# Kernel optimization log

Hardware: AMD Instinct MI355X
Metric: run time of the kernel (lower is better)

## Reference

```python
import jax, jax.numpy as jnp
import numpy as np

D_MODEL = 1024
N_HEADS = 16
D_K = D_MODEL // N_HEADS


def setup_inputs() -> dict:
    key = jax.random.key(0)
    ks = jax.random.split(key, 5)
    s = 1.0 / np.sqrt(D_MODEL)
    x = jax.random.normal(ks[0], (4, 2048, D_MODEL), dtype=jnp.float32)
    W_qkv = jax.random.normal(ks[1], (D_MODEL, 3 * D_MODEL), dtype=jnp.float32) * s
    b_qkv = jnp.zeros((3 * D_MODEL,), dtype=jnp.float32)
    W_proj = jax.random.normal(ks[2], (D_MODEL, D_MODEL), dtype=jnp.float32) * s
    b_proj = jnp.zeros((D_MODEL,), dtype=jnp.float32)
    return {"x": x, "W_qkv": W_qkv, "b_qkv": b_qkv, "W_proj": W_proj, "b_proj": b_proj}


def reference(x, W_qkv, b_qkv, W_proj, b_proj):
    B, T, C = x.shape
    qkv = x @ W_qkv + b_qkv  # [B,T,3C]
    q, k, v = jnp.split(qkv, 3, axis=2)
    # [B,T,C] -> [B,H,T,dk]
    def to_heads(t):
        return t.reshape(B, T, N_HEADS, D_K).transpose(0, 2, 1, 3)
    q, k, v = to_heads(q), to_heads(k), to_heads(v)
    scale = 1.0 / np.sqrt(D_K)
    att = jnp.einsum('bhqd,bhkd->bhqk', q, k) * scale
    causal = jnp.tril(jnp.ones((T, T), dtype=bool))
    att = jnp.where(causal, att, -jnp.inf)
    att = jax.nn.softmax(att, axis=-1)
    y = jnp.einsum('bhqk,bhkd->bhqd', att, v)
    y = y.transpose(0, 2, 1, 3).reshape(B, T, C)
    return y @ W_proj + b_proj
```

## Files before the change

### kernel.cpp

```cpp
#include <hip/hip_runtime.h>
#include <stdint.h>


typedef float  floatx4 __attribute__((ext_vector_type(4)));
typedef __bf16 bf16x8  __attribute__((ext_vector_type(8)));
typedef __bf16 bf16x4  __attribute__((ext_vector_type(4)));

#define AS1 __attribute__((address_space(1)))
#define AS3 __attribute__((address_space(3)))

__device__ __forceinline__ void gload_lds16(const void* g, void* l) {
    __builtin_amdgcn_global_load_lds((AS1 void*)(uintptr_t)g,
                                     (AS3 void*)(uintptr_t)l, 16, 0, 0);
}

#if __has_builtin(__builtin_amdgcn_exp2f)
#define EXP2F(x) __builtin_amdgcn_exp2f(x)
#else
#define EXP2F(x) exp2f(x)
#endif

#define LOG2E 1.44269504088896340736f
#define ATT_SC (0.125f * LOG2E)
#define MASK_NEG (-3.0e4f)

static constexpr int Bn = 4, Tn = 2048, Cn = 1024, Hn = 16, DKn = 64;
static constexpr int BT = Bn * Tn;
static constexpr int N_QKV = 3 * Cn;
static constexpr int PAD = 68;


__global__ void cast_x_kernel(const float* __restrict__ x, __bf16* __restrict__ xb, int n) {
    int i = (blockIdx.x * blockDim.x + threadIdx.x) * 4;
    if (i < n) {
        float4 v = *(const float4*)(x + i);
        bf16x4 o;
        o[0] = (__bf16)v.x; o[1] = (__bf16)v.y; o[2] = (__bf16)v.z; o[3] = (__bf16)v.w;
        *(bf16x4*)(xb + i) = o;
    }
}

__global__ void transpose_cast_kernel(const float* __restrict__ W, __bf16* __restrict__ WT,
                                      int R, int C) {
    __shared__ float tile[32][33];
    int tx = threadIdx.x & 31, ty = threadIdx.x >> 5;
    int r0 = blockIdx.y * 32, c0 = blockIdx.x * 32;
#pragma unroll
    for (int i = 0; i < 4; i++)
        tile[ty + i * 8][tx] = W[(size_t)(r0 + ty + i * 8) * C + c0 + tx];
    __syncthreads();
#pragma unroll
    for (int i = 0; i < 4; i++)
        WT[(size_t)(c0 + ty + i * 8) * R + r0 + tx] = (__bf16)tile[tx][ty + i * 8];
}

__global__ __launch_bounds__(256) void gemm_qkv_kernel(
    const __bf16* __restrict__ A, const __bf16* __restrict__ Bt,
    const float* __restrict__ bias,
    __bf16* __restrict__ Qo, __bf16* __restrict__ Ko, __bf16* __restrict__ Vo) {
    const int K = 1024;
    __shared__ __bf16 Al[128 * 32];
    __shared__ __bf16 Bl[128 * 32];
    int tid = threadIdx.x, w = tid >> 6, lane = tid & 63;
    int lq = lane >> 4, l16 = lane & 15;
    int bm = blockIdx.y, bn = blockIdx.x;
    int wm = w & 1, wn = w >> 1;

    const __bf16* Ag = A + (size_t)(bm * 128 + w * 32 + (lane >> 2)) * K + (lane & 3) * 8;
    const __bf16* Bg = Bt + (size_t)(bn * 128 + w * 32 + (lane >> 2)) * K + (lane & 3) * 8;
    __bf16* AlW = Al + w * 32 * 32;
    __bf16* BlW = Bl + w * 32 * 32;

    floatx4 acc[4][4] = {};
    for (int k0 = 0; k0 < K; k0 += 32) {
        __syncthreads();
        gload_lds16(Ag + k0, AlW);
        gload_lds16(Ag + k0 + 16 * K, AlW + 16 * 32);
        gload_lds16(Bg + k0, BlW);
        gload_lds16(Bg + k0 + 16 * K, BlW + 16 * 32);
        __syncthreads();
        bf16x8 af[4], bf[4];
#pragma unroll
        for (int i = 0; i < 4; i++)
            af[i] = *(const bf16x8*)&Al[(wm * 64 + i * 16 + l16) * 32 + lq * 8];
#pragma unroll
        for (int i = 0; i < 4; i++)
            bf[i] = *(const bf16x8*)&Bl[(wn * 64 + i * 16 + l16) * 32 + lq * 8];
#pragma unroll
        for (int mt = 0; mt < 4; mt++)
#pragma unroll
            for (int nt = 0; nt < 4; nt++)
                acc[mt][nt] = __builtin_amdgcn_mfma_f32_16x16x32_bf16(
                    af[mt], bf[nt], acc[mt][nt], 0, 0, 0);
    }
#pragma unroll
    for (int nt = 0; nt < 4; nt++) {
        int gbase = bn * 128 + wn * 64 + nt * 16;
        int gcol = gbase + l16;
        int which = gbase >> 10;
        float bv = bias[gcol];
        if (which == 2) {
            int hh = (gbase - 2048) >> 6;
            int dd = ((gbase - 2048) & 63) + l16;
#pragma unroll
            for (int mt = 0; mt < 4; mt++) {
                int growb = bm * 128 + wm * 64 + mt * 16 + lq * 4;
                int bb = growb >> 11, tt = growb & 2047;
                bf16x4 v4;
#pragma unroll
                for (int r = 0; r < 4; r++) v4[r] = (__bf16)(acc[mt][nt][r] + bv);
                *(bf16x4*)&Vo[((size_t)(bb * 16 + hh) * 64 + dd) * 2048 + tt] = v4;
            }
        } else {
            int rem = gbase & 1023;
            int hh = rem >> 6, dd = (rem & 63) + l16;
            __bf16* dst = (which == 0) ? Qo : Ko;
            float scl = (which == 0) ? ATT_SC : 1.0f;
#pragma unroll
            for (int mt = 0; mt < 4; mt++) {
#pragma unroll
                for (int r = 0; r < 4; r++) {
                    int grow = bm * 128 + wm * 64 + mt * 16 + lq * 4 + r;
                    int bb = grow >> 11, tt = grow & 2047;
                    dst[((size_t)(bb * 16 + hh) * 2048 + tt) * 64 + dd] =
                        (__bf16)((acc[mt][nt][r] + bv) * scl);
                }
            }
        }
    }
}

__global__ __launch_bounds__(256) void gemm_proj_kernel(
    const __bf16* __restrict__ A, const __bf16* __restrict__ Bt,
    const float* __restrict__ bias, float* __restrict__ out) {
    const int K = 1024;
    __shared__ __bf16 Al[128 * 32];
    __shared__ __bf16 Bl[128 * 32];
    int tid = threadIdx.x, w = tid >> 6, lane = tid & 63;
    int lq = lane >> 4, l16 = lane & 15;
    int bm = blockIdx.y, bn = blockIdx.x;
    int wm = w & 1, wn = w >> 1;

    const __bf16* Ag = A + (size_t)(bm * 128 + w * 32 + (lane >> 2)) * K + (lane & 3) * 8;
    const __bf16* Bg = Bt + (size_t)(bn * 128 + w * 32 + (lane >> 2)) * K + (lane & 3) * 8;
    __bf16* AlW = Al + w * 32 * 32;
    __bf16* BlW = Bl + w * 32 * 32;

    floatx4 acc[4][4] = {};
    for (int k0 = 0; k0 < K; k0 += 32) {
        __syncthreads();
        gload_lds16(Ag + k0, AlW);
        gload_lds16(Ag + k0 + 16 * K, AlW + 16 * 32);
        gload_lds16(Bg + k0, BlW);
        gload_lds16(Bg + k0 + 16 * K, BlW + 16 * 32);
        __syncthreads();
        bf16x8 af[4], bf[4];
#pragma unroll
        for (int i = 0; i < 4; i++)
            af[i] = *(const bf16x8*)&Al[(wm * 64 + i * 16 + l16) * 32 + lq * 8];
#pragma unroll
        for (int i = 0; i < 4; i++)
            bf[i] = *(const bf16x8*)&Bl[(wn * 64 + i * 16 + l16) * 32 + lq * 8];
#pragma unroll
        for (int mt = 0; mt < 4; mt++)
#pragma unroll
            for (int nt = 0; nt < 4; nt++)
                acc[mt][nt] = __builtin_amdgcn_mfma_f32_16x16x32_bf16(
                    af[mt], bf[nt], acc[mt][nt], 0, 0, 0);
    }
#pragma unroll
    for (int nt = 0; nt < 4; nt++) {
        int gcol = bn * 128 + wn * 64 + nt * 16 + l16;
        float bv = bias[gcol];
#pragma unroll
        for (int mt = 0; mt < 4; mt++) {
#pragma unroll
            for (int r = 0; r < 4; r++) {
                int grow = bm * 128 + wm * 64 + mt * 16 + lq * 4 + r;
                out[(size_t)grow * 1024 + gcol] = acc[mt][nt][r] + bv;
            }
        }
    }
}

__global__ __launch_bounds__(256) void attn_kernel(
    const __bf16* __restrict__ Q, const __bf16* __restrict__ K,
    const __bf16* __restrict__ Vt, __bf16* __restrict__ Y) {
    const int bid = blockIdx.x;
    const int pr = bid >> 6, bh = bid & 63;
    const int b = bh >> 4, h = bh & 15;
    int tid = threadIdx.x, w = tid >> 6, lane = tid & 63;
    int lq = lane >> 4, l16 = lane & 15;

    const __bf16* Qh = Q + (size_t)bh * Tn * DKn;
    const __bf16* Kh = K + (size_t)bh * Tn * DKn;
    const __bf16* Vh = Vt + (size_t)bh * DKn * Tn;

    __shared__ __bf16 Kl[64 * PAD];
    __shared__ __bf16 Vl[64 * PAD];
    __shared__ __bf16 Pl[128 * PAD];

    int srow = tid >> 3, ssl = tid & 7;

    bf16x8 onesf;
#pragma unroll
    for (int j = 0; j < 8; j++) onesf[j] = (__bf16)1.0f;

    bf16x8 kr0 = *(const bf16x8*)&Kh[(size_t)srow * 64 + ssl * 8];
    bf16x8 kr1 = *(const bf16x8*)&Kh[(size_t)(srow + 32) * 64 + ssl * 8];
    bf16x8 vr0 = *(const bf16x8*)&Vh[(size_t)srow * 2048 + ssl * 8];
    bf16x8 vr1 = *(const bf16x8*)&Vh[(size_t)(srow + 32) * 2048 + ssl * 8];

#pragma unroll
    for (int seg = 0; seg < 2; seg++) {
        const int qt = seg ? (15 - pr) : pr;
        const int q0 = qt * 128;
        const int ktmax = 2 * qt + 1;

        bf16x8 qf[2][2];
#pragma unroll
        for (int mt = 0; mt < 2; mt++)
#pragma unroll
            for (int ks = 0; ks < 2; ks++)
                qf[mt][ks] = *(const bf16x8*)&Qh[(size_t)(q0 + w * 32 + mt * 16 + l16) * 64 +
                                                 ks * 32 + lq * 8];

        floatx4 oacc[2][5] = {};

        for (int kt = 0; kt <= ktmax; kt++) {
            __syncthreads();
            *(bf16x8*)&Kl[srow * PAD + ssl * 8] = kr0;
            *(bf16x8*)&Kl[(srow + 32) * PAD + ssl * 8] = kr1;
            *(bf16x8*)&Vl[srow * PAD + ssl * 8] = vr0;
            *(bf16x8*)&Vl[(srow + 32) * PAD + ssl * 8] = vr1;
            __syncthreads();
            if (!(seg == 1 && kt == ktmax)) {
                int nk = (kt < ktmax) ? (kt + 1) : 0;
                kr0 = *(const bf16x8*)&Kh[(size_t)(nk * 64 + srow) * 64 + ssl * 8];
                kr1 = *(const bf16x8*)&Kh[(size_t)(nk * 64 + srow + 32) * 64 + ssl * 8];
                vr0 = *(const bf16x8*)&Vh[(size_t)srow * 2048 + nk * 64 + ssl * 8];
                vr1 = *(const bf16x8*)&Vh[(size_t)(srow + 32) * 2048 + nk * 64 + ssl * 8];
            }

            floatx4 s2[2][4] = {};
#pragma unroll
            for (int ks = 0; ks < 2; ks++) {
                bf16x8 kf[4];
#pragma unroll
                for (int nt = 0; nt < 4; nt++)
                    kf[nt] = *(const bf16x8*)&Kl[(nt * 16 + l16) * PAD + ks * 32 + lq * 8];
#pragma unroll
                for (int mt = 0; mt < 2; mt++)
#pragma unroll
                    for (int nt = 0; nt < 4; nt++)
                        s2[mt][nt] = __builtin_amdgcn_mfma_f32_16x16x32_bf16(
                            qf[mt][ks], kf[nt], s2[mt][nt], 0, 0, 0);
            }

            if (kt >= 2 * qt) {
#pragma unroll
                for (int mt = 0; mt < 2; mt++)
#pragma unroll
                    for (int nt = 0; nt < 4; nt++) {
                        int col = kt * 64 + nt * 16 + l16;
#pragma unroll
                        for (int r = 0; r < 4; r++) {
                            int row = q0 + w * 32 + mt * 16 + lq * 4 + r;
                            if (col > row) s2[mt][nt][r] = MASK_NEG;
                        }
                    }
            }

#pragma unroll
            for (int mt = 0; mt < 2; mt++) {
#pragma unroll
                for (int nt = 0; nt < 4; nt++) {
#pragma unroll
                    for (int r = 0; r < 4; r++) {
                        float p = EXP2F(s2[mt][nt][r]);
                        int rowl = w * 32 + mt * 16 + lq * 4 + r;
                        Pl[rowl * PAD + nt * 16 + l16] = (__bf16)p;
                    }
                }
            }

#pragma unroll
            for (int ks = 0; ks < 2; ks++) {
                bf16x8 pf[2], vf[4];
#pragma unroll
                for (int mt = 0; mt < 2; mt++)
                    pf[mt] = *(const bf16x8*)&Pl[(w * 32 + mt * 16 + l16) * PAD + ks * 32 + lq * 8];
#pragma unroll
                for (int dt = 0; dt < 4; dt++)
                    vf[dt] = *(const bf16x8*)&Vl[(dt * 16 + l16) * PAD + ks * 32 + lq * 8];
#pragma unroll
                for (int mt = 0; mt < 2; mt++) {
#pragma unroll
                    for (int dt = 0; dt < 4; dt++)
                        oacc[mt][dt] = __builtin_amdgcn_mfma_f32_16x16x32_bf16(
                            pf[mt], vf[dt], oacc[mt][dt], 0, 0, 0);
                    oacc[mt][4] = __builtin_amdgcn_mfma_f32_16x16x32_bf16(
                        pf[mt], onesf, oacc[mt][4], 0, 0, 0);
                }
            }
        }

#pragma unroll
        for (int mt = 0; mt < 2; mt++) {
#pragma unroll
            for (int r = 0; r < 4; r++) {
                float inv = 1.0f / oacc[mt][4][r];
                int rowg = q0 + w * 32 + mt * 16 + lq * 4 + r;
#pragma unroll
                for (int dt = 0; dt < 4; dt++)
                    Y[((size_t)(b * 2048 + rowg)) * 1024 + h * 64 + dt * 16 + l16] =
                        (__bf16)(oacc[mt][dt][r] * inv);
            }
        }
    }
}


extern "C" void kernel_launch(void* const* d_in, const int* in_sizes, int n_in,
                              void* d_out, int out_size, void* d_ws, size_t ws_size,
                              hipStream_t stream) {
    const float* x     = (const float*)d_in[0];
    const float* Wqkv  = (const float*)d_in[1];
    const float* bqkv  = (const float*)d_in[2];
    const float* Wproj = (const float*)d_in[3];
    const float* bproj = (const float*)d_in[4];
    float* out = (float*)d_out;

    __bf16* xb     = (__bf16*)d_ws;
    __bf16* WqkvT  = xb + (size_t)BT * Cn;
    __bf16* WprojT = WqkvT + (size_t)N_QKV * Cn;
    __bf16* Qb     = WprojT + (size_t)Cn * Cn;
    __bf16* Kb     = Qb + (size_t)BT * Cn;
    __bf16* Vb     = Kb + (size_t)BT * Cn;
    __bf16* Yb     = Vb + (size_t)BT * Cn;

    int nx = BT * Cn;
    cast_x_kernel<<<(nx / 4 + 255) / 256, 256, 0, stream>>>(x, xb, nx);
    transpose_cast_kernel<<<dim3(N_QKV / 32, Cn / 32), 256, 0, stream>>>(Wqkv, WqkvT, Cn, N_QKV);
    transpose_cast_kernel<<<dim3(Cn / 32, Cn / 32), 256, 0, stream>>>(Wproj, WprojT, Cn, Cn);

    gemm_qkv_kernel<<<dim3(N_QKV / 128, BT / 128), 256, 0, stream>>>(
        xb, WqkvT, bqkv, Qb, Kb, Vb);

    attn_kernel<<<dim3(512), 256, 0, stream>>>(Qb, Kb, Vb, Yb);

    gemm_proj_kernel<<<dim3(Cn / 128, BT / 128), 256, 0, stream>>>(
        Yb, WprojT, bproj, out);
}
```

Baseline: 260.7 us.

## Double-buffer K/V tiles in LDS and drop a barrier per attention step

K and V tiles now go to a two-slot LDS buffer: the next tile is written into the other slot while the current slot feeds the MFMAs, so each step needs one barrier instead of two. A flat tile counter with a KTILE mapping prefetches across both causal segments. The exp/P-store is split per k-slice to interleave with the PV MFMAs, and s_setprio raises wave priority around the MFMA bursts. It costs twice the LDS for K/V, which may reduce occupancy.

```diff
diff --git a/kernel.cpp b/kernel.cpp
--- a/kernel.cpp
+++ b/kernel.cpp
@@ -196,8 +196,8 @@
     const __bf16* Kh = K + (size_t)bh * Tn * DKn;
     const __bf16* Vh = Vt + (size_t)bh * DKn * Tn;
 
-    __shared__ __bf16 Kl[64 * PAD];
-    __shared__ __bf16 Vl[64 * PAD];
+    __shared__ __bf16 Kl[2][64 * PAD];
+    __shared__ __bf16 Vl[2][64 * PAD];
     __shared__ __bf16 Pl[128 * PAD];
 
     int srow = tid >> 3, ssl = tid & 7;
@@ -205,12 +205,29 @@
     bf16x8 onesf;
 #pragma unroll
     for (int j = 0; j < 8; j++) onesf[j] = (__bf16)1.0f;
+
+    const int km0 = 2 * pr + 1;
+    const int NT = 34;
+
+#define KTILE(ff) ((ff) <= km0 ? (ff) : (ff) - km0 - 1)
 
     bf16x8 kr0 = *(const bf16x8*)&Kh[(size_t)srow * 64 + ssl * 8];
     bf16x8 kr1 = *(const bf16x8*)&Kh[(size_t)(srow + 32) * 64 + ssl * 8];
     bf16x8 vr0 = *(const bf16x8*)&Vh[(size_t)srow * 2048 + ssl * 8];
     bf16x8 vr1 = *(const bf16x8*)&Vh[(size_t)(srow + 32) * 2048 + ssl * 8];
-
+    *(bf16x8*)&Kl[0][srow * PAD + ssl * 8] = kr0;
+    *(bf16x8*)&Kl[0][(srow + 32) * PAD + ssl * 8] = kr1;
+    *(bf16x8*)&Vl[0][srow * PAD + ssl * 8] = vr0;
+    *(bf16x8*)&Vl[0][(srow + 32) * PAD + ssl * 8] = vr1;
+    {
+        int nk = KTILE(1);
+        kr0 = *(const bf16x8*)&Kh[(size_t)(nk * 64 + srow) * 64 + ssl * 8];
+        kr1 = *(const bf16x8*)&Kh[(size_t)(nk * 64 + srow + 32) * 64 + ssl * 8];
+        vr0 = *(const bf16x8*)&Vh[(size_t)srow * 2048 + nk * 64 + ssl * 8];
+        vr1 = *(const bf16x8*)&Vh[(size_t)(srow + 32) * 2048 + nk * 64 + ssl * 8];
+    }
+
+    int par = 0, f = 0;
 #pragma unroll
     for (int seg = 0; seg < 2; seg++) {
         const int qt = seg ? (15 - pr) : pr;
@@ -227,20 +244,26 @@
 
         floatx4 oacc[2][5] = {};
 
-        for (int kt = 0; kt <= ktmax; kt++) {
+        for (int kt = 0; kt <= ktmax; kt++, f++) {
             __syncthreads();
-            *(bf16x8*)&Kl[srow * PAD + ssl * 8] = kr0;
-            *(bf16x8*)&Kl[(srow + 32) * PAD + ssl * 8] = kr1;
-            *(bf16x8*)&Vl[srow * PAD + ssl * 8] = vr0;
-            *(bf16x8*)&Vl[(srow + 32) * PAD + ssl * 8] = vr1;
-            __syncthreads();
-            if (!(seg == 1 && kt == ktmax)) {
-                int nk = (kt < ktmax) ? (kt + 1) : 0;
-                kr0 = *(const bf16x8*)&Kh[(size_t)(nk * 64 + srow) * 64 + ssl * 8];
-                kr1 = *(const bf16x8*)&Kh[(size_t)(nk * 64 + srow + 32) * 64 + ssl * 8];
-                vr0 = *(const bf16x8*)&Vh[(size_t)srow * 2048 + nk * 64 + ssl * 8];
-                vr1 = *(const bf16x8*)&Vh[(size_t)(srow + 32) * 2048 + nk * 64 + ssl * 8];
-            }
+            if (f + 1 < NT) {
+                __bf16* Kn = &Kl[par ^ 1][0];
+                __bf16* Vn = &Vl[par ^ 1][0];
+                *(bf16x8*)&Kn[srow * PAD + ssl * 8] = kr0;
+                *(bf16x8*)&Kn[(srow + 32) * PAD + ssl * 8] = kr1;
+                *(bf16x8*)&Vn[srow * PAD + ssl * 8] = vr0;
+                *(bf16x8*)&Vn[(srow + 32) * PAD + ssl * 8] = vr1;
+                if (f + 2 < NT) {
+                    int nk = KTILE(f + 2);
+                    kr0 = *(const bf16x8*)&Kh[(size_t)(nk * 64 + srow) * 64 + ssl * 8];
+                    kr1 = *(const bf16x8*)&Kh[(size_t)(nk * 64 + srow + 32) * 64 + ssl * 8];
+                    vr0 = *(const bf16x8*)&Vh[(size_t)srow * 2048 + nk * 64 + ssl * 8];
+                    vr1 = *(const bf16x8*)&Vh[(size_t)(srow + 32) * 2048 + nk * 64 + ssl * 8];
+                }
+            }
+
+            const __bf16* Kc = &Kl[par][0];
+            const __bf16* Vc = &Vl[par][0];
 
             floatx4 s2[2][4] = {};
 #pragma unroll
@@ -248,13 +271,15 @@
                 bf16x8 kf[4];
 #pragma unroll
                 for (int nt = 0; nt < 4; nt++)
-                    kf[nt] = *(const bf16x8*)&Kl[(nt * 16 + l16) * PAD + ks * 32 + lq * 8];
+                    kf[nt] = *(const bf16x8*)&Kc[(nt * 16 + l16) * PAD + ks * 32 + lq * 8];
+                __builtin_amdgcn_s_setprio(1);
 #pragma unroll
                 for (int mt = 0; mt < 2; mt++)
 #pragma unroll
                     for (int nt = 0; nt < 4; nt++)
                         s2[mt][nt] = __builtin_amdgcn_mfma_f32_16x16x32_bf16(
                             qf[mt][ks], kf[nt], s2[mt][nt], 0, 0, 0);
+                __builtin_amdgcn_s_setprio(0);
             }
 
             if (kt >= 2 * qt) {
@@ -272,27 +297,28 @@
             }
 
 #pragma unroll
-            for (int mt = 0; mt < 2; mt++) {
-#pragma unroll
-                for (int nt = 0; nt < 4; nt++) {
-#pragma unroll
-                    for (int r = 0; r < 4; r++) {
-                        float p = EXP2F(s2[mt][nt][r]);
-                        int rowl = w * 32 + mt * 16 + lq * 4 + r;
-                        Pl[rowl * PAD + nt * 16 + l16] = (__bf16)p;
+            for (int ks = 0; ks < 2; ks++) {
+#pragma unroll
+                for (int mt = 0; mt < 2; mt++) {
+#pragma unroll
+                    for (int nth = 0; nth < 2; nth++) {
+                        int nt = ks * 2 + nth;
+#pragma unroll
+                        for (int r = 0; r < 4; r++) {
+                            float p = EXP2F(s2[mt][nt][r]);
+                            int rowl = w * 32 + mt * 16 + lq * 4 + r;
+                            Pl[rowl * PAD + nt * 16 + l16] = (__bf16)p;
+                        }
                     }
                 }
-            }
-
-#pragma unroll
-            for (int ks = 0; ks < 2; ks++) {
                 bf16x8 pf[2], vf[4];
 #pragma unroll
                 for (int mt = 0; mt < 2; mt++)
                     pf[mt] = *(const bf16x8*)&Pl[(w * 32 + mt * 16 + l16) * PAD + ks * 32 + lq * 8];
 #pragma unroll
                 for (int dt = 0; dt < 4; dt++)
-                    vf[dt] = *(const bf16x8*)&Vl[(dt * 16 + l16) * PAD + ks * 32 + lq * 8];
+                    vf[dt] = *(const bf16x8*)&Vc[(dt * 16 + l16) * PAD + ks * 32 + lq * 8];
+                __builtin_amdgcn_s_setprio(1);
 #pragma unroll
                 for (int mt = 0; mt < 2; mt++) {
 #pragma unroll
@@ -302,7 +328,9 @@
                     oacc[mt][4] = __builtin_amdgcn_mfma_f32_16x16x32_bf16(
                         pf[mt], onesf, oacc[mt][4], 0, 0, 0);
                 }
-            }
+                __builtin_amdgcn_s_setprio(0);
+            }
+            par ^= 1;
         }
 
 #pragma unroll
@@ -318,6 +346,7 @@
             }
         }
     }
+#undef KTILE
 }
 
 
```

New measurement: 352.2 us. 1.35x slower.
